# Performance work log

Measured on AMD Instinct MI355X. Metric: run time of the kernel, lower is better.

The kernel has to match this reference:

```python
import jax, jax.numpy as jnp
import numpy as np

B, N, D = 256, 256, 256
DELTA_BEARING = 5.0
DELTA_HEADING = 5.0
N_HEAD = int(360 / DELTA_HEADING)   # 72
N_BEAR = int(360 / DELTA_BEARING)   # 72
DOMAIN_PARAM = 2.0
EPS = 1e-14


def setup_inputs() -> dict:
    key = jax.random.key(0)
    ks = jax.random.split(key, 8)
    hidden_state = jax.random.normal(ks[0], (B, N, D), dtype=jnp.float32)
    distance_matrix = jax.random.uniform(ks[1], (B, N, N), dtype=jnp.float32) * 10.0
    bearing_matrix = jax.random.uniform(ks[2], (B, N, N), dtype=jnp.float32) * 360.0
    heading_matrix = jax.random.uniform(ks[3], (B, N, N), dtype=jnp.float32) * 360.0
    sequence_mask = (jax.random.uniform(ks[4], (B, N)) > 0.1).astype(jnp.float32)
    domain = jnp.full((N_HEAD, N_BEAR), DOMAIN_PARAM, dtype=jnp.float32)
    lim = 1.0 / np.sqrt(2 * D)
    W = jax.random.uniform(ks[5], (D, 2 * D), minval=-lim, maxval=lim, dtype=jnp.float32)
    b = jax.random.uniform(ks[6], (D,), minval=-lim, maxval=lim, dtype=jnp.float32)
    return {"hidden_state": hidden_state, "distance_matrix": distance_matrix,
            "bearing_matrix": bearing_matrix, "heading_matrix": heading_matrix,
            "sequence_mask": sequence_mask, "domain": domain, "W": W, "b": b}


def _compute_weights(domain, distance_matrix, bearing_matrix, heading_matrix, sequence_mask):
    # domain lookup indices from heading/bearing bins
    idx1 = jnp.clip(jnp.floor((heading_matrix + DELTA_HEADING / 2) / DELTA_HEADING), 0, N_HEAD - 1).astype(jnp.int32)
    idx2 = jnp.clip(jnp.floor((bearing_matrix + DELTA_BEARING / 2) / DELTA_BEARING), 0, N_BEAR - 1).astype(jnp.int32)
    w = jax.nn.relu(domain[idx1, idx2] - distance_matrix)  # (B,N,N)
    # pairwise sequence mask and no-self-attention mask
    wm = sequence_mask[:, :, None] * sequence_mask[:, None, :]  # (B,N,N)
    ped = 1.0 - jnp.eye(w.shape[1], dtype=w.dtype)               # (N,N)
    valid = (ped[None, :, :] * wm) > 0
    w = jnp.where(valid, w, 0.0)
    # masked softmax over dim=2: zeros are treated as masked, epsilon-stabilized
    mask = (w != 0).astype(w.dtype)
    masked_exps = jnp.exp(w) * mask + EPS
    w = masked_exps / (masked_exps.sum(axis=2, keepdims=True) + EPS)
    return jnp.where(valid, w, 0.0)


def reference(hidden_state, distance_matrix, bearing_matrix, heading_matrix, sequence_mask, domain, W, b):
    weights = _compute_weights(domain, distance_matrix, bearing_matrix, heading_matrix, sequence_mask)
    weighted_hidden = jnp.einsum('bij,bjd->bid', weights, hidden_state)  # (B,N,D)
    cat = jnp.concatenate([weighted_hidden, hidden_state], axis=-1)       # (B,N,2D)
    return jnp.einsum('bnk,dk->bnd', cat, W) + b
```

## Files before the change

### kernel.cpp

```cpp
#include <hip/hip_runtime.h>
#include <hip/hip_bf16.h>


typedef __attribute__((ext_vector_type(4))) float  f32x4;
typedef __attribute__((ext_vector_type(8))) short  bf16x8;
typedef __attribute__((ext_vector_type(4))) short  bf16x4;

#define EPSC 1e-14f

__device__ __forceinline__ short f2bf(float v) {
  __hip_bfloat16 h = __float2bfloat16(v);
  return *reinterpret_cast<short*>(&h);
}

__global__ void k0_pack(const float* __restrict__ W, short* __restrict__ Wbf) {
  int idx = blockIdx.x * 256 + threadIdx.x;
  f32x4 v = *(const f32x4*)(W + (size_t)idx * 4);
  bf16x4 pk;
  pk[0] = f2bf(v[0]); pk[1] = f2bf(v[1]); pk[2] = f2bf(v[2]); pk[3] = f2bf(v[3]);
  *(bf16x4*)(Wbf + (size_t)idx * 4) = pk;
}

__global__ void k0_check(const float* __restrict__ domain, float* __restrict__ flag) {
  __shared__ int s_ok[4];
  const int t = threadIdx.x;
  float v0 = domain[0];
  bool ok = true;
  for (int x = t; x < 72 * 72; x += 256) ok = ok && (domain[x] == v0);
  unsigned long long m = __ballot(ok);
  if ((t & 63) == 0) s_ok[t >> 6] = (m == ~0ull) ? 1 : 0;
  __syncthreads();
  if (t == 0) {
    flag[0] = v0;
    flag[1] = (s_ok[0] && s_ok[1] && s_ok[2] && s_ok[3]) ? 1.f : 0.f;
  }
}

__global__ __launch_bounds__(512) void k1_proj(
    const float* __restrict__ H, const short* __restrict__ Wbf,
    short* __restrict__ P1T) {
  extern __shared__ char sm[];
  char* sA = sm;
  char* sB = sm + 9216;
  const int t  = threadIdx.x;
  const int n0 = blockIdx.x * 64;
  const int b  = n0 >> 8;
  const int jb = n0 & 255;

  const int wid = t >> 6, l = t & 63;
  const int wn = wid >> 2, wc = wid & 3;
  const int lr = l & 15, lg = l >> 4;
  f32x4 acc[2][4] = {};

  for (int kk = 0; kk < 256; kk += 64) {
    __syncthreads();
    #pragma unroll
    for (int p = 0; p < 2; ++p) {
      int q = t + 512 * p;
      int j = q >> 4, seg = q & 15;
      f32x4 hv = *(const f32x4*)(H + ((size_t)(n0 + j)) * 256 + kk + seg * 4);
      bf16x4 pk;
      pk[0] = f2bf(hv[0]); pk[1] = f2bf(hv[1]); pk[2] = f2bf(hv[2]); pk[3] = f2bf(hv[3]);
      *(bf16x4*)(sA + j * 144 + seg * 8) = pk;
    }
    #pragma unroll
    for (int p = 0; p < 4; ++p) {
      int z = t + 512 * p;
      int d = z >> 3, s = z & 7;
      bf16x8 v = *(const bf16x8*)(Wbf + (size_t)d * 512 + kk + s * 8);
      *(bf16x8*)(sB + d * 144 + s * 16) = v;
    }
    __syncthreads();
    #pragma unroll
    for (int sub = 0; sub < 2; ++sub) {
      bf16x8 a[2], bb[4];
      #pragma unroll
      for (int m = 0; m < 2; ++m) {
        int row = wn * 32 + m * 16 + lr;
        a[m] = *(const bf16x8*)(sA + row * 144 + sub * 64 + lg * 16);
      }
      #pragma unroll
      for (int f = 0; f < 4; ++f) {
        int d = wc * 64 + f * 16 + lr;
        bb[f] = *(const bf16x8*)(sB + d * 144 + sub * 64 + lg * 16);
      }
      #pragma unroll
      for (int m = 0; m < 2; ++m) {
        #pragma unroll
        for (int f = 0; f < 4; ++f)
          acc[m][f] = __builtin_amdgcn_mfma_f32_16x16x32_bf16(a[m], bb[f], acc[m][f], 0, 0, 0);
      }
    }
  }

  #pragma unroll
  for (int m = 0; m < 2; ++m) {
    int jl = wn * 32 + m * 16 + lg * 4;
    #pragma unroll
    for (int f = 0; f < 4; ++f) {
      int d = wc * 64 + f * 16 + lr;
      f32x4 v = acc[m][f];
      bf16x4 pk;
      pk[0] = f2bf(v[0]); pk[1] = f2bf(v[1]); pk[2] = f2bf(v[2]); pk[3] = f2bf(v[3]);
      *(bf16x4*)(P1T + (size_t)b * 65536 + (size_t)d * 256 + jb + jl) = pk;
    }
  }
}

__global__ __launch_bounds__(256) void k2a_weights(
    const float* __restrict__ dist, const float* __restrict__ bear,
    const float* __restrict__ head, const float* __restrict__ seqmask,
    const float* __restrict__ domain, const float* __restrict__ uflag,
    short* __restrict__ weBuf) {
  __shared__ float sMask[256];
  const int t = threadIdx.x;
  const int b = blockIdx.x >> 3;
  const int i0 = (blockIdx.x & 7) * 32;
  if (t < 256) sMask[t] = seqmask[b * 256 + t];
  __syncthreads();

  const int w = t >> 6, l = t & 63;
  const int j0 = l * 4;
  const float dval = uflag[0];
  const bool  uni  = uflag[1] != 0.f;
  const f32x4 mj = *(const f32x4*)(sMask + j0);

  f32x4 dv[8];
  #pragma unroll
  for (int rr = 0; rr < 8; ++rr) {
    int i = i0 + w * 8 + rr;
    dv[rr] = *(const f32x4*)(dist + ((size_t)b * 256 + i) * 256 + j0);
  }

  #pragma unroll
  for (int rr = 0; rr < 8; ++rr) {
    const int i = i0 + w * 8 + rr;
    const float mI = sMask[i];
    const size_t base = ((size_t)b * 256 + i) * 256;
    float ev[4];
    float rs = 0.f;
    if (uni) {
      #pragma unroll
      for (int e = 0; e < 4; ++e) {
        float wv = fmaxf(dval - dv[rr][e], 0.f);
        bool valid = (i != j0 + e) && (mI != 0.f) && (mj[e] != 0.f);
        float ex = (wv > 0.f) ? __expf(wv) : 0.f;
        ex = valid ? ex : 0.f;
        rs += ex;
        ev[e] = valid ? (ex + EPSC) : 0.f;
      }
    } else {
      f32x4 bv = *(const f32x4*)(bear + base + j0);
      f32x4 hv = *(const f32x4*)(head + base + j0);
      #pragma unroll
      for (int e = 0; e < 4; ++e) {
        float f1 = fminf(fmaxf(floorf((hv[e] + 2.5f) * 0.2f), 0.f), 71.f);
        float f2 = fminf(fmaxf(floorf((bv[e] + 2.5f) * 0.2f), 0.f), 71.f);
        float wv = fmaxf(domain[(int)(f1 * 72.f + f2)] - dv[rr][e], 0.f);
        bool valid = (i != j0 + e) && (mI != 0.f) && (mj[e] != 0.f);
        float ex = (wv > 0.f) ? __expf(wv) : 0.f;
        ex = valid ? ex : 0.f;
        rs += ex;
        ev[e] = valid ? (ex + EPSC) : 0.f;
      }
    }
    rs += __shfl_xor(rs, 1, 64);
    rs += __shfl_xor(rs, 2, 64);
    rs += __shfl_xor(rs, 4, 64);
    rs += __shfl_xor(rs, 8, 64);
    rs += __shfl_xor(rs, 16, 64);
    rs += __shfl_xor(rs, 32, 64);
    const float scale = 1.0f / (rs + 257.0f * EPSC);
    bf16x4 pk;
    pk[0] = f2bf(ev[0] * scale); pk[1] = f2bf(ev[1] * scale);
    pk[2] = f2bf(ev[2] * scale); pk[3] = f2bf(ev[3] * scale);
    *(bf16x4*)(weBuf + base + j0) = pk;
  }
}

__global__ __launch_bounds__(512) void k2b_gemm(
    const short* __restrict__ weBuf, const float* __restrict__ H,
    const short* __restrict__ P1T, const short* __restrict__ Wbf,
    const float* __restrict__ bias, float* __restrict__ out) {
  extern __shared__ char sm[];
  char*  sA    = sm;
  char*  sB    = sm + 18432;
  float* sBias = (float*)(sm + 18432 + 36864);
  const int t  = threadIdx.x;
  const int b  = blockIdx.x >> 1;
  const int i0 = (blockIdx.x & 1) * 128;

  if (t < 256) sBias[t] = bias[t];

  const int wid = t >> 6, l = t & 63;
  const int wm = wid >> 1, wn = wid & 1;
  const int lr = l & 15, lg = l >> 4;
  f32x4 acc[2][8] = {};

  for (int kk = 0; kk < 512; kk += 64) {
    __syncthreads();
    if (kk < 256) {
      #pragma unroll
      for (int p = 0; p < 2; ++p) {
        int z = t + 512 * p;
        int row = z >> 3, s = z & 7;
        bf16x8 v = *(const bf16x8*)(weBuf + ((size_t)b * 256 + i0 + row) * 256 + kk + s * 8);
        *(bf16x8*)(sA + row * 144 + s * 16) = v;
      }
    } else {
      #pragma unroll
      for (int p = 0; p < 2; ++p) {
        int z = t + 512 * p;
        int row = z >> 3, s = z & 7;
        const float* src = H + ((size_t)b * 256 + i0 + row) * 256 + (kk - 256) + s * 8;
        f32x4 h0 = *(const f32x4*)(src);
        f32x4 h1 = *(const f32x4*)(src + 4);
        bf16x8 pk;
        pk[0] = f2bf(h0[0]); pk[1] = f2bf(h0[1]); pk[2] = f2bf(h0[2]); pk[3] = f2bf(h0[3]);
        pk[4] = f2bf(h1[0]); pk[5] = f2bf(h1[1]); pk[6] = f2bf(h1[2]); pk[7] = f2bf(h1[3]);
        *(bf16x8*)(sA + row * 144 + s * 16) = pk;
      }
    }
    #pragma unroll
    for (int p = 0; p < 4; ++p) {
      int z = t + 512 * p;
      int d = z >> 3, s = z & 7;
      bf16x8 v;
      if (kk < 256) v = *(const bf16x8*)(P1T + (size_t)b * 65536 + (size_t)d * 256 + kk + s * 8);
      else          v = *(const bf16x8*)(Wbf + (size_t)d * 512 + kk + s * 8);
      *(bf16x8*)(sB + d * 144 + s * 16) = v;
    }
    __syncthreads();
    #pragma unroll
    for (int sub = 0; sub < 2; ++sub) {
      bf16x8 a[2], bb[8];
      #pragma unroll
      for (int m = 0; m < 2; ++m) {
        int row = wm * 32 + m * 16 + lr;
        a[m] = *(const bf16x8*)(sA + row * 144 + sub * 64 + lg * 16);
      }
      #pragma unroll
      for (int n = 0; n < 8; ++n) {
        int d = wn * 128 + n * 16 + lr;
        bb[n] = *(const bf16x8*)(sB + d * 144 + sub * 64 + lg * 16);
      }
      #pragma unroll
      for (int m = 0; m < 2; ++m) {
        #pragma unroll
        for (int n = 0; n < 8; ++n)
          acc[m][n] = __builtin_amdgcn_mfma_f32_16x16x32_bf16(a[m], bb[n], acc[m][n], 0, 0, 0);
      }
    }
  }

  #pragma unroll
  for (int m = 0; m < 2; ++m) {
    int rl = wm * 32 + m * 16 + lg * 4;
    #pragma unroll
    for (int n = 0; n < 8; ++n) {
      int d = wn * 128 + n * 16 + lr;
      float bs = sBias[d];
      #pragma unroll
      for (int r = 0; r < 4; ++r) {
        int row = rl + r;
        out[((size_t)b * 256 + i0 + row) * 256 + d] = acc[m][n][r] + bs;
      }
    }
  }
}

extern "C" void kernel_launch(void* const* d_in, const int* in_sizes, int n_in,
                              void* d_out, int out_size, void* d_ws, size_t ws_size,
                              hipStream_t stream) {
  const float* hidden  = (const float*)d_in[0];
  const float* dist    = (const float*)d_in[1];
  const float* bear    = (const float*)d_in[2];
  const float* head    = (const float*)d_in[3];
  const float* seqmask = (const float*)d_in[4];
  const float* domain  = (const float*)d_in[5];
  const float* W       = (const float*)d_in[6];
  const float* bias    = (const float*)d_in[7];
  float* out = (float*)d_out;

  char* ws = (char*)d_ws;
  short* Wbf   = (short*)ws;
  float* flag  = (float*)(ws + 524288);
  short* P1T   = (short*)(ws + (1u << 20));
  short* weBuf = (short*)(ws + (1u << 20) + (32u << 20));

  k0_pack<<<128, 256, 0, stream>>>(W, Wbf);
  k0_check<<<1, 256, 0, stream>>>(domain, flag);
  k1_proj<<<1024, 512, 46080, stream>>>(hidden, Wbf, P1T);
  k2a_weights<<<2048, 256, 0, stream>>>(dist, bear, head, seqmask, domain, flag, weBuf);
  k2b_gemm<<<512, 512, 56320, stream>>>(weBuf, hidden, P1T, Wbf, bias, out);
}
```

Before: 113.6 us.

## Merge projection and softmax-weight kernels; precompute H·W2+bias to halve final GEMM

The projection and attention-weight kernels are merged into one launch, with blocks specialized by index range. The projection blocks now also compute the hidden-state half of the output projection plus bias and store it as a bf16 buffer. The final GEMM then covers only K=256 (weights × P1T): the P1T tile is loaded straight into LDS with global_load_lds and an XOR swizzle, A fragments are read directly from global memory, and the precomputed bf16 partial is added in the epilogue. This removes one launch and the second fp32 read of H, in exchange for an extra 32MB bf16 intermediate, scattered 2-byte stores, and added rounding error from storing that partial in bf16.

Result: slower. 118.7 us (+4.5%).

```diff
diff --git a/kernel.cpp b/kernel.cpp
--- a/kernel.cpp
+++ b/kernel.cpp
@@ -11,6 +11,14 @@
 __device__ __forceinline__ short f2bf(float v) {
   __hip_bfloat16 h = __float2bfloat16(v);
   return *reinterpret_cast<short*>(&h);
+}
+__device__ __forceinline__ float bf2f(unsigned short u) {
+  union { unsigned int i; float f; } c; c.i = ((unsigned int)u) << 16; return c.f;
+}
+__device__ __forceinline__ void gload16(const void* g, void* l) {
+  __builtin_amdgcn_global_load_lds(
+      (const __attribute__((address_space(1))) void*)g,
+      (__attribute__((address_space(3))) void*)l, 16, 0, 0);
 }
 
 __global__ void k0_pack(const float* __restrict__ W, short* __restrict__ Wbf) {
@@ -36,235 +44,224 @@
   }
 }
 
-__global__ __launch_bounds__(512) void k1_proj(
+__global__ __launch_bounds__(512) void kA(
     const float* __restrict__ H, const short* __restrict__ Wbf,
-    short* __restrict__ P1T) {
+    const float* __restrict__ bias, const float* __restrict__ dist,
+    const float* __restrict__ bear, const float* __restrict__ head,
+    const float* __restrict__ seqmask, const float* __restrict__ domain,
+    const float* __restrict__ uflag,
+    short* __restrict__ P1T, short* __restrict__ P2, short* __restrict__ weBuf) {
   extern __shared__ char sm[];
-  char* sA = sm;
-  char* sB = sm + 9216;
-  const int t  = threadIdx.x;
-  const int n0 = blockIdx.x * 64;
-  const int b  = n0 >> 8;
-  const int jb = n0 & 255;
-
-  const int wid = t >> 6, l = t & 63;
-  const int wn = wid >> 2, wc = wid & 3;
-  const int lr = l & 15, lg = l >> 4;
-  f32x4 acc[2][4] = {};
-
-  for (int kk = 0; kk < 256; kk += 64) {
-    __syncthreads();
-    #pragma unroll
-    for (int p = 0; p < 2; ++p) {
-      int q = t + 512 * p;
-      int j = q >> 4, seg = q & 15;
-      f32x4 hv = *(const f32x4*)(H + ((size_t)(n0 + j)) * 256 + kk + seg * 4);
-      bf16x4 pk;
-      pk[0] = f2bf(hv[0]); pk[1] = f2bf(hv[1]); pk[2] = f2bf(hv[2]); pk[3] = f2bf(hv[3]);
-      *(bf16x4*)(sA + j * 144 + seg * 8) = pk;
-    }
+  const int t = threadIdx.x;
+
+  if (blockIdx.x < 1024) {
+    char* sA = sm;
+    char* sB = sm + 33792;
+    const int n0 = blockIdx.x * 64;
+    const int b  = n0 >> 8;
+    const int jb = n0 & 255;
+
     #pragma unroll
     for (int p = 0; p < 4; ++p) {
       int z = t + 512 * p;
-      int d = z >> 3, s = z & 7;
-      bf16x8 v = *(const bf16x8*)(Wbf + (size_t)d * 512 + kk + s * 8);
-      *(bf16x8*)(sB + d * 144 + s * 16) = v;
-    }
+      int j = z >> 5, seg = z & 31;
+      const float* src = H + (size_t)(n0 + j) * 256 + seg * 8;
+      f32x4 h0 = *(const f32x4*)src;
+      f32x4 h1 = *(const f32x4*)(src + 4);
+      bf16x8 pk;
+      pk[0] = f2bf(h0[0]); pk[1] = f2bf(h0[1]); pk[2] = f2bf(h0[2]); pk[3] = f2bf(h0[3]);
+      pk[4] = f2bf(h1[0]); pk[5] = f2bf(h1[1]); pk[6] = f2bf(h1[2]); pk[7] = f2bf(h1[3]);
+      *(bf16x8*)(sA + j * 528 + seg * 16) = pk;
+    }
+
+    const int wid = t >> 6, l = t & 63;
+    const int wn = wid >> 2, wc = wid & 3;
+    const int lr = l & 15, lg = l >> 4;
+
+    #pragma unroll
+    for (int pass = 0; pass < 2; ++pass) {
+      f32x4 acc[2][4] = {};
+      for (int kk = 0; kk < 256; kk += 64) {
+        __syncthreads();
+        #pragma unroll
+        for (int p = 0; p < 4; ++p) {
+          int z = t + 512 * p;
+          int d = z >> 3, s = z & 7;
+          bf16x8 v = *(const bf16x8*)(Wbf + (size_t)d * 512 + pass * 256 + kk + s * 8);
+          *(bf16x8*)(sB + d * 144 + s * 16) = v;
+        }
+        __syncthreads();
+        #pragma unroll
+        for (int sub = 0; sub < 2; ++sub) {
+          bf16x8 a[2], bb[4];
+          #pragma unroll
+          for (int m = 0; m < 2; ++m) {
+            int row = wn * 32 + m * 16 + lr;
+            a[m] = *(const bf16x8*)(sA + row * 528 + (kk + sub * 32 + lg * 8) * 2);
+          }
+          #pragma unroll
+          for (int f = 0; f < 4; ++f) {
+            int d = wc * 64 + f * 16 + lr;
+            bb[f] = *(const bf16x8*)(sB + d * 144 + sub * 64 + lg * 16);
+          }
+          #pragma unroll
+          for (int m = 0; m < 2; ++m) {
+            #pragma unroll
+            for (int f = 0; f < 4; ++f)
+              acc[m][f] = __builtin_amdgcn_mfma_f32_16x16x32_bf16(a[m], bb[f], acc[m][f], 0, 0, 0);
+          }
+        }
+      }
+      if (pass == 0) {
+        #pragma unroll
+        for (int m = 0; m < 2; ++m) {
+          int jl = wn * 32 + m * 16 + lg * 4;
+          #pragma unroll
+          for (int f = 0; f < 4; ++f) {
+            int d = wc * 64 + f * 16 + lr;
+            f32x4 v = acc[m][f];
+            bf16x4 pk;
+            pk[0] = f2bf(v[0]); pk[1] = f2bf(v[1]); pk[2] = f2bf(v[2]); pk[3] = f2bf(v[3]);
+            *(bf16x4*)(P1T + (size_t)b * 65536 + (size_t)d * 256 + jb + jl) = pk;
+          }
+        }
+      } else {
+        #pragma unroll
+        for (int m = 0; m < 2; ++m) {
+          int jl = wn * 32 + m * 16 + lg * 4;
+          #pragma unroll
+          for (int f = 0; f < 4; ++f) {
+            int d = wc * 64 + f * 16 + lr;
+            float bs = bias[d];
+            f32x4 v = acc[m][f];
+            #pragma unroll
+            for (int r = 0; r < 4; ++r)
+              P2[(size_t)b * 65536 + (size_t)(jb + jl + r) * 256 + d] = f2bf(v[r] + bs);
+          }
+        }
+      }
+    }
+  } else {
+    float* sMask = (float*)sm;
+    const int idx = blockIdx.x - 1024;
+    const int b  = idx >> 2;
+    const int i0 = (idx & 3) * 64;
+    if (t < 256) sMask[t] = seqmask[b * 256 + t];
     __syncthreads();
+
+    const int w = t >> 6, l = t & 63;
+    const int j0 = l * 4;
+    const float dval = uflag[0];
+    const bool  uni  = uflag[1] != 0.f;
+    const f32x4 mj = *(const f32x4*)(sMask + j0);
+
+    f32x4 dv[8];
+    #pragma unroll
+    for (int rr = 0; rr < 8; ++rr) {
+      int i = i0 + w * 8 + rr;
+      dv[rr] = *(const f32x4*)(dist + ((size_t)b * 256 + i) * 256 + j0);
+    }
+
+    #pragma unroll
+    for (int rr = 0; rr < 8; ++rr) {
+      const int i = i0 + w * 8 + rr;
+      const float mI = sMask[i];
+      const size_t base = ((size_t)b * 256 + i) * 256;
+      float ev[4];
+      float rs = 0.f;
+      if (uni) {
+        #pragma unroll
+        for (int e = 0; e < 4; ++e) {
+          float wv = fmaxf(dval - dv[rr][e], 0.f);
+          bool valid = (i != j0 + e) && (mI != 0.f) && (mj[e] != 0.f);
+          float ex = (wv > 0.f) ? __expf(wv) : 0.f;
+          ex = valid ? ex : 0.f;
+          rs += ex;
+          ev[e] = valid ? (ex + EPSC) : 0.f;
+        }
+      } else {
+        f32x4 bv = *(const f32x4*)(bear + base + j0);
+        f32x4 hv = *(const f32x4*)(head + base + j0);
+        #pragma unroll
+        for (int e = 0; e < 4; ++e) {
+          float f1 = fminf(fmaxf(floorf((hv[e] + 2.5f) * 0.2f), 0.f), 71.f);
+          float f2 = fminf(fmaxf(floorf((bv[e] + 2.5f) * 0.2f), 0.f), 71.f);
+          float wv = fmaxf(domain[(int)(f1 * 72.f + f2)] - dv[rr][e], 0.f);
+          bool valid = (i != j0 + e) && (mI != 0.f) && (mj[e] != 0.f);
+          float ex = (wv > 0.f) ? __expf(wv) : 0.f;
+          ex = valid ? ex : 0.f;
+          rs += ex;
+          ev[e] = valid ? (ex + EPSC) : 0.f;
+        }
+      }
+      rs += __shfl_xor(rs, 1, 64);
+      rs += __shfl_xor(rs, 2, 64);
+      rs += __shfl_xor(rs, 4, 64);
+      rs += __shfl_xor(rs, 8, 64);
+      rs += __shfl_xor(rs, 16, 64);
+      rs += __shfl_xor(rs, 32, 64);
+      const float scale = 1.0f / (rs + 257.0f * EPSC);
+      bf16x4 pk;
+      pk[0] = f2bf(ev[0] * scale); pk[1] = f2bf(ev[1] * scale);
+      pk[2] = f2bf(ev[2] * scale); pk[3] = f2bf(ev[3] * scale);
+      *(bf16x4*)(weBuf + base + j0) = pk;
+    }
+  }
+}
+
+__global__ __launch_bounds__(512) void k2b_gemm(
+    const short* __restrict__ weBuf, const short* __restrict__ P1T,
+    const short* __restrict__ P2, float* __restrict__ out) {
+  extern __shared__ char sm[];
+  char* sB = sm;
+  const int t = threadIdx.x;
+  const int x = blockIdx.x;
+  const int blk = (x & 7) * 128 + (x >> 3);
+  const int b  = blk >> 2;
+  const int i0 = (blk & 3) * 64;
+
+  const int wid = t >> 6, l = t & 63;
+  const int lr = l & 15, lg = l >> 4;
+  const int wr = wid & 3, wc = wid >> 2;
+  const int r3 = l >> 3, sl = l & 7;
+  const int sswz = (sl ^ r3) * 8;
+  const int sw = (lr & 7) << 4;
+
+  const short* __restrict__ P1b = P1T + (size_t)b * 65536;
+  const int i = i0 + wr * 16 + lr;
+  const size_t abase = ((size_t)b * 256 + i) * 256;
+
+  f32x4 acc[8] = {};
+
+  for (int c = 0; c < 4; ++c) {
+    const int kk = c * 64;
+    #pragma unroll
+    for (int p = 0; p < 4; ++p) {
+      int dd = wid * 8 + r3 + 64 * p;
+      gload16(P1b + (size_t)dd * 256 + kk + sswz, sB + (wid * 8 + 64 * p) * 128);
+    }
+    __syncthreads();
     #pragma unroll
     for (int sub = 0; sub < 2; ++sub) {
-      bf16x8 a[2], bb[4];
-      #pragma unroll
-      for (int m = 0; m < 2; ++m) {
-        int row = wn * 32 + m * 16 + lr;
-        a[m] = *(const bf16x8*)(sA + row * 144 + sub * 64 + lg * 16);
-      }
-      #pragma unroll
-      for (int f = 0; f < 4; ++f) {
-        int d = wc * 64 + f * 16 + lr;
-        bb[f] = *(const bf16x8*)(sB + d * 144 + sub * 64 + lg * 16);
-      }
-      #pragma unroll
-      for (int m = 0; m < 2; ++m) {
-        #pragma unroll
-        for (int f = 0; f < 4; ++f)
-          acc[m][f] = __builtin_amdgcn_mfma_f32_16x16x32_bf16(a[m], bb[f], acc[m][f], 0, 0, 0);
-      }
-    }
-  }
-
-  #pragma unroll
-  for (int m = 0; m < 2; ++m) {
-    int jl = wn * 32 + m * 16 + lg * 4;
-    #pragma unroll
-    for (int f = 0; f < 4; ++f) {
-      int d = wc * 64 + f * 16 + lr;
-      f32x4 v = acc[m][f];
-      bf16x4 pk;
-      pk[0] = f2bf(v[0]); pk[1] = f2bf(v[1]); pk[2] = f2bf(v[2]); pk[3] = f2bf(v[3]);
-      *(bf16x4*)(P1T + (size_t)b * 65536 + (size_t)d * 256 + jb + jl) = pk;
-    }
-  }
-}
-
-__global__ __launch_bounds__(256) void k2a_weights(
-    const float* __restrict__ dist, const float* __restrict__ bear,
-    const float* __restrict__ head, const float* __restrict__ seqmask,
-    const float* __restrict__ domain, const float* __restrict__ uflag,
-    short* __restrict__ weBuf) {
-  __shared__ float sMask[256];
-  const int t = threadIdx.x;
-  const int b = blockIdx.x >> 3;
-  const int i0 = (blockIdx.x & 7) * 32;
-  if (t < 256) sMask[t] = seqmask[b * 256 + t];
-  __syncthreads();
-
-  const int w = t >> 6, l = t & 63;
-  const int j0 = l * 4;
-  const float dval = uflag[0];
-  const bool  uni  = uflag[1] != 0.f;
-  const f32x4 mj = *(const f32x4*)(sMask + j0);
-
-  f32x4 dv[8];
-  #pragma unroll
-  for (int rr = 0; rr < 8; ++rr) {
-    int i = i0 + w * 8 + rr;
-    dv[rr] = *(const f32x4*)(dist + ((size_t)b * 256 + i) * 256 + j0);
-  }
-
-  #pragma unroll
-  for (int rr = 0; rr < 8; ++rr) {
-    const int i = i0 + w * 8 + rr;
-    const float mI = sMask[i];
-    const size_t base = ((size_t)b * 256 + i) * 256;
-    float ev[4];
-    float rs = 0.f;
-    if (uni) {
-      #pragma unroll
-      for (int e = 0; e < 4; ++e) {
-        float wv = fmaxf(dval - dv[rr][e], 0.f);
-        bool valid = (i != j0 + e) && (mI != 0.f) && (mj[e] != 0.f);
-        float ex = (wv > 0.f) ? __expf(wv) : 0.f;
-        ex = valid ? ex : 0.f;
-        rs += ex;
-        ev[e] = valid ? (ex + EPSC) : 0.f;
-      }
-    } else {
-      f32x4 bv = *(const f32x4*)(bear + base + j0);
-      f32x4 hv = *(const f32x4*)(head + base + j0);
-      #pragma unroll
-      for (int e = 0; e < 4; ++e) {
-        float f1 = fminf(fmaxf(floorf((hv[e] + 2.5f) * 0.2f), 0.f), 71.f);
-        float f2 = fminf(fmaxf(floorf((bv[e] + 2.5f) * 0.2f), 0.f), 71.f);
-        float wv = fmaxf(domain[(int)(f1 * 72.f + f2)] - dv[rr][e], 0.f);
-        bool valid = (i != j0 + e) && (mI != 0.f) && (mj[e] != 0.f);
-        float ex = (wv > 0.f) ? __expf(wv) : 0.f;
-        ex = valid ? ex : 0.f;
-        rs += ex;
-        ev[e] = valid ? (ex + EPSC) : 0.f;
-      }
-    }
-    rs += __shfl_xor(rs, 1, 64);
-    rs += __shfl_xor(rs, 2, 64);
-    rs += __shfl_xor(rs, 4, 64);
-    rs += __shfl_xor(rs, 8, 64);
-    rs += __shfl_xor(rs, 16, 64);
-    rs += __shfl_xor(rs, 32, 64);
-    const float scale = 1.0f / (rs + 257.0f * EPSC);
-    bf16x4 pk;
-    pk[0] = f2bf(ev[0] * scale); pk[1] = f2bf(ev[1] * scale);
-    pk[2] = f2bf(ev[2] * scale); pk[3] = f2bf(ev[3] * scale);
-    *(bf16x4*)(weBuf + base + j0) = pk;
-  }
-}
-
-__global__ __launch_bounds__(512) void k2b_gemm(
-    const short* __restrict__ weBuf, const float* __restrict__ H,
-    const short* __restrict__ P1T, const short* __restrict__ Wbf,
-    const float* __restrict__ bias, float* __restrict__ out) {
-  extern __shared__ char sm[];
-  char*  sA    = sm;
-  char*  sB    = sm + 18432;
-  float* sBias = (float*)(sm + 18432 + 36864);
-  const int t  = threadIdx.x;
-  const int b  = blockIdx.x >> 1;
-  const int i0 = (blockIdx.x & 1) * 128;
-
-  if (t < 256) sBias[t] = bias[t];
-
-  const int wid = t >> 6, l = t & 63;
-  const int wm = wid >> 1, wn = wid & 1;
-  const int lr = l & 15, lg = l >> 4;
-  f32x4 acc[2][8] = {};
-
-  for (int kk = 0; kk < 512; kk += 64) {
-    __syncthreads();
-    if (kk < 256) {
-      #pragma unroll
-      for (int p = 0; p < 2; ++p) {
-        int z = t + 512 * p;
-        int row = z >> 3, s = z & 7;
-        bf16x8 v = *(const bf16x8*)(weBuf + ((size_t)b * 256 + i0 + row) * 256 + kk + s * 8);
-        *(bf16x8*)(sA + row * 144 + s * 16) = v;
-      }
-    } else {
-      #pragma unroll
-      for (int p = 0; p < 2; ++p) {
-        int z = t + 512 * p;
-        int row = z >> 3, s = z & 7;
-        const float* src = H + ((size_t)b * 256 + i0 + row) * 256 + (kk - 256) + s * 8;
-        f32x4 h0 = *(const f32x4*)(src);
-        f32x4 h1 = *(const f32x4*)(src + 4);
-        bf16x8 pk;
-        pk[0] = f2bf(h0[0]); pk[1] = f2bf(h0[1]); pk[2] = f2bf(h0[2]); pk[3] = f2bf(h0[3]);
-        pk[4] = f2bf(h1[0]); pk[5] = f2bf(h1[1]); pk[6] = f2bf(h1[2]); pk[7] = f2bf(h1[3]);
-        *(bf16x8*)(sA + row * 144 + s * 16) = pk;
-      }
-    }
-    #pragma unroll
-    for (int p = 0; p < 4; ++p) {
-      int z = t + 512 * p;
-      int d = z >> 3, s = z & 7;
-      bf16x8 v;
-      if (kk < 256) v = *(const bf16x8*)(P1T + (size_t)b * 65536 + (size_t)d * 256 + kk + s * 8);
-      else          v = *(const bf16x8*)(Wbf + (size_t)d * 512 + kk + s * 8);
-      *(bf16x8*)(sB + d * 144 + s * 16) = v;
-    }
-    __syncthreads();
-    #pragma unroll
-    for (int sub = 0; sub < 2; ++sub) {
-      bf16x8 a[2], bb[8];
-      #pragma unroll
-      for (int m = 0; m < 2; ++m) {
-        int row = wm * 32 + m * 16 + lr;
-        a[m] = *(const bf16x8*)(sA + row * 144 + sub * 64 + lg * 16);
-      }
+      bf16x8 av = *(const bf16x8*)(weBuf + abase + kk + sub * 32 + lg * 8);
       #pragma unroll
       for (int n = 0; n < 8; ++n) {
-        int d = wn * 128 + n * 16 + lr;
-        bb[n] = *(const bf16x8*)(sB + d * 144 + sub * 64 + lg * 16);
-      }
-      #pragma unroll
-      for (int m = 0; m < 2; ++m) {
-        #pragma unroll
-        for (int n = 0; n < 8; ++n)
-          acc[m][n] = __builtin_amdgcn_mfma_f32_16x16x32_bf16(a[m], bb[n], acc[m][n], 0, 0, 0);
-      }
-    }
+        const int d = wc * 128 + n * 16 + lr;
+        bf16x8 bb = *(const bf16x8*)(sB + d * 128 + ((sub * 64 + lg * 16) ^ sw));
+        acc[n] = __builtin_amdgcn_mfma_f32_16x16x32_bf16(av, bb, acc[n], 0, 0, 0);
+      }
+    }
+    __syncthreads();
   }
 
   #pragma unroll
-  for (int m = 0; m < 2; ++m) {
-    int rl = wm * 32 + m * 16 + lg * 4;
-    #pragma unroll
-    for (int n = 0; n < 8; ++n) {
-      int d = wn * 128 + n * 16 + lr;
-      float bs = sBias[d];
-      #pragma unroll
-      for (int r = 0; r < 4; ++r) {
-        int row = rl + r;
-        out[((size_t)b * 256 + i0 + row) * 256 + d] = acc[m][n][r] + bs;
-      }
+  for (int n = 0; n < 8; ++n) {
+    const int d = wc * 128 + n * 16 + lr;
+    #pragma unroll
+    for (int r = 0; r < 4; ++r) {
+      const int row = i0 + wr * 16 + lg * 4 + r;
+      const size_t off = ((size_t)b * 256 + row) * 256 + d;
+      out[off] = acc[n][r] + bf2f((unsigned short)P2[off]);
     }
   }
 }
@@ -286,11 +283,12 @@
   short* Wbf   = (short*)ws;
   float* flag  = (float*)(ws + 524288);
   short* P1T   = (short*)(ws + (1u << 20));
-  short* weBuf = (short*)(ws + (1u << 20) + (32u << 20));
+  short* P2    = (short*)(ws + (1u << 20) + (32u << 20));
+  short* weBuf = (short*)(ws + (1u << 20) + (64u << 20));
 
   k0_pack<<<128, 256, 0, stream>>>(W, Wbf);
   k0_check<<<1, 256, 0, stream>>>(domain, flag);
-  k1_proj<<<1024, 512, 46080, stream>>>(hidden, Wbf, P1T);
-  k2a_weights<<<2048, 256, 0, stream>>>(dist, bear, head, seqmask, domain, flag, weBuf);
-  k2b_gemm<<<512, 512, 56320, stream>>>(weBuf, hidden, P1T, Wbf, bias, out);
-}
+  kA<<<2048, 512, 70656, stream>>>(hidden, Wbf, bias, dist, bear, head,
+                                   seqmask, domain, flag, P1T, P2, weBuf);
+  k2b_gemm<<<1024, 512, 32768, stream>>>(weBuf, P1T, P2, out);
+}
```
